# Performance work log

Measured on AMD Instinct MI355X. Metric: run time of the kernel, lower is better.

Reference implementation:

```python
import jax, jax.numpy as jnp
import numpy as np

CNT_R = 500
DIM = 128
B, NEI = 8192, 64


def setup_inputs() -> dict:
    key = jax.random.key(0)
    ks = jax.random.split(key, 10)
    d2 = 2 * DIM
    return {
        "batch_nei_e_emb": jax.random.normal(ks[0], (B, NEI, DIM), dtype=jnp.float32),
        "batch_nei_rw": jax.random.uniform(ks[1], (B, NEI), dtype=jnp.float32),
        "w_r_table": jax.random.normal(ks[2], (2 * CNT_R + 1, DIM), dtype=jnp.float32),
        "zq_table": jax.random.normal(ks[3], (2 * CNT_R, DIM), dtype=jnp.float32),
        "attn_W_w": jax.random.normal(ks[4], (d2, d2), dtype=jnp.float32) / np.sqrt(d2),
        "attn_W_b": jnp.zeros((d2,), dtype=jnp.float32),
        "u_a_w": jax.random.normal(ks[5], (d2,), dtype=jnp.float32) / np.sqrt(d2),
        "u_a_b": jnp.zeros((), dtype=jnp.float32),
        "batch_nei_rid": jax.random.randint(ks[6], (B, NEI), 0, 2 * CNT_R + 1),
        "batch_q_rid": jax.random.randint(ks[7], (B,), 0, 2 * CNT_R),
    }


def reference(batch_nei_e_emb, batch_nei_rw, w_r_table, zq_table,
              attn_W_w, attn_W_b, u_a_w, u_a_b,
              batch_nei_rid, batch_q_rid):
    # gather relation hyperplane normals: (B, NEI, DIM)
    w_r = w_r_table[batch_nei_rid]
    n = w_r / jnp.linalg.norm(w_r, axis=-1, keepdims=True)
    # hyperplane projection: e - (e . n) n
    e = batch_nei_e_emb
    e_proj = e - jnp.sum(e * n, axis=-1, keepdims=True) * n
    # query relation embedding, tiled over neighbors: (B, NEI, DIM)
    z_q = zq_table[batch_q_rid]  # (B, DIM)
    z_q = jnp.broadcast_to(z_q[:, None, :], e_proj.shape)
    concat = jnp.concatenate([z_q, e_proj], axis=-1)  # (B, NEI, 2*DIM)
    h = jnp.tanh(jnp.einsum('bni,oi->bno', concat, attn_W_w) + attn_W_b)
    _alpha = jnp.einsum('bni,i->bn', h, u_a_w) + u_a_b  # (B, NEI)
    alpha = jax.nn.softmax(_alpha, axis=-1)
    attn = alpha + batch_nei_rw
    return attn
```

## Files before the change

### kernel.cpp

```cpp
#include <hip/hip_runtime.h>
#include <hip/hip_bf16.h>

#define NB    8192
#define NEI   64
#define DIM   128
#define D2    256
#define NR_W  1001
#define NR_Z  1000
#define EPB_LD 136
#define BPB   2
#define C2L2E 2.8853900817779268f

typedef __attribute__((ext_vector_type(8))) short bf16x8;
typedef __attribute__((ext_vector_type(4))) float f32x4;

__device__ __forceinline__ ushort f2bf(float x) {
    union { float f; unsigned u; } c; c.f = x;
    unsigned u = c.u;
    return (ushort)((u + 0x7fffu + ((u >> 16) & 1u)) >> 16);
}

__device__ __forceinline__ unsigned pk2(float a, float b) {
    __hip_bfloat162 h = __float22bfloat162_rn(make_float2(a, b));
    return *(unsigned*)&h;
}


__global__ void k_norm(const float* __restrict__ w_r_table, float* __restrict__ norm_t) {
    int r = blockIdx.x;
    int t = threadIdx.x;
    float v = w_r_table[r * DIM + t];
    float s = v * v;
    #pragma unroll
    for (int m = 1; m < 64; m <<= 1) s += __shfl_xor(s, m);
    __shared__ float sh[2];
    if ((t & 63) == 0) sh[t >> 6] = s;
    __syncthreads();
    float tot = sh[0] + sh[1];
    norm_t[r * DIM + t] = v / sqrtf(tot);
}

__global__ void k_tq(const float* __restrict__ zq_table, const float* __restrict__ W,
                     const float* __restrict__ bias, float* __restrict__ tq_t) {
    int r = blockIdx.x;
    int o = threadIdx.x;
    __shared__ float4 z4[32];
    if (o < 32) z4[o] = ((const float4*)(zq_table + r * DIM))[o];
    __syncthreads();
    const float4* wr = (const float4*)(W + o * D2);
    float acc = bias[o];
    #pragma unroll 8
    for (int i = 0; i < 32; ++i) {
        float4 wv = wr[i], zv = z4[i];
        acc += wv.x*zv.x + wv.y*zv.y + wv.z*zv.z + wv.w*zv.w;
    }
    tq_t[r * D2 + o] = acc;
}

__global__ void k_bfrag(const float* __restrict__ W, ushort* __restrict__ bfrag) {
    int ot = blockIdx.x;
    int kt = blockIdx.y;
    int l  = threadIdx.x;
    int o  = ot * 16 + (l & 15);
    int k  = kt * 32 + (l >> 4) * 8;
    const float4* src = (const float4*)(W + o * D2 + DIM + k);
    float4 a = src[0], c = src[1];
    uint4 w;
    w.x = f2bf(a.x) | ((unsigned)f2bf(a.y) << 16);
    w.y = f2bf(a.z) | ((unsigned)f2bf(a.w) << 16);
    w.z = f2bf(c.x) | ((unsigned)f2bf(c.y) << 16);
    w.w = f2bf(c.z) | ((unsigned)f2bf(c.w) << 16);
    *(uint4*)(bfrag + ((ot * 4 + kt) * 64 + l) * 8) = w;
}

__global__ void k_sua(const float* __restrict__ u, float* __restrict__ sua) {
    int t = threadIdx.x;
    float v = u[t];
    #pragma unroll
    for (int m = 1; m < 64; m <<= 1) v += __shfl_xor(v, m);
    __shared__ float sh[4];
    if ((t & 63) == 0) sh[t >> 6] = v;
    __syncthreads();
    if (t == 0) sua[0] = sh[0] + sh[1] + sh[2] + sh[3];
}


__global__ __launch_bounds__(512, 4) void k_main(
    const float* __restrict__ e_emb,
    const float* __restrict__ rw,
    const int*   __restrict__ nei_rid,
    const int*   __restrict__ q_rid,
    const float* __restrict__ norm_t,
    const float* __restrict__ tq_t,
    const ushort* __restrict__ bfrag,
    const float* __restrict__ u_a_sum,
    const float* __restrict__ u_a_w,
    float* __restrict__ out)
{
    __shared__ __align__(16) ushort ep16[NEI * EPB_LD];
    __shared__ float alpw[8][NEI];

    const int t    = threadIdx.x;
    const int wave = t >> 6, lane = t & 63;
    const int ln   = lane & 15, hi = lane >> 4;
    const int row  = t >> 3, q3 = t & 7;
    const int b0   = blockIdx.x * BPB;

    bf16x8 bfr_[2][4];
    #pragma unroll
    for (int nt = 0; nt < 2; ++nt)
        #pragma unroll
        for (int kt = 0; kt < 4; ++kt)
            bfr_[nt][kt] = *(const bf16x8*)(bfrag + ((((wave*2+nt)*4 + kt)*64 + lane)*8));
    asm volatile("" : "+v"(bfr_[0][0]), "+v"(bfr_[0][1]), "+v"(bfr_[0][2]), "+v"(bfr_[0][3]),
                      "+v"(bfr_[1][0]), "+v"(bfr_[1][1]), "+v"(bfr_[1][2]), "+v"(bfr_[1][3]));
    float ua2[2];
    #pragma unroll
    for (int nt = 0; nt < 2; ++nt) ua2[nt] = u_a_w[wave*32 + nt*16 + ln];
    asm volatile("" : "+v"(ua2[0]), "+v"(ua2[1]));
    const float sua = u_a_sum[0];

    #pragma unroll 1
    for (int i = 0; i < BPB; ++i) {
        const int b = b0 + i;

        {
            const int rid = nei_rid[b * NEI + row];
            const float4* esrc = (const float4*)(e_emb + ((size_t)b * NEI + row) * DIM);
            const float4* nsrc = (const float4*)(norm_t + rid * DIM);
            float4 ev[4], nv[4];
            #pragma unroll
            for (int kk = 0; kk < 4; ++kk) {
                ev[kk] = esrc[q3 + 8*kk];
                nv[kk] = nsrc[q3 + 8*kk];
            }
            float part = 0.f;
            #pragma unroll
            for (int kk = 0; kk < 4; ++kk)
                part += ev[kk].x*nv[kk].x + ev[kk].y*nv[kk].y + ev[kk].z*nv[kk].z + ev[kk].w*nv[kk].w;
            part += __shfl_xor(part, 1);
            part += __shfl_xor(part, 2);
            part += __shfl_xor(part, 4);
            const float d = part;
            #pragma unroll
            for (int kk = 0; kk < 4; ++kk) {
                float p0 = fmaf(-d, nv[kk].x, ev[kk].x);
                float p1 = fmaf(-d, nv[kk].y, ev[kk].y);
                float p2 = fmaf(-d, nv[kk].z, ev[kk].z);
                float p3 = fmaf(-d, nv[kk].w, ev[kk].w);
                uint2 w2; w2.x = pk2(p0, p1); w2.y = pk2(p2, p3);
                *(uint2*)((char*)ep16 + row * (EPB_LD*2) + (q3 + 8*kk) * 8) = w2;
            }
        }

        float tq2[2];
        {
            int qr = q_rid[b];
            #pragma unroll
            for (int nt = 0; nt < 2; ++nt)
                tq2[nt] = C2L2E * tq_t[qr * D2 + wave*32 + nt*16 + ln];
        }

        __syncthreads();

        #pragma unroll
        for (int mt = 0; mt < 4; ++mt) {
            bf16x8 a_[4];
            #pragma unroll
            for (int kt = 0; kt < 4; ++kt)
                a_[kt] = *(const bf16x8*)&ep16[(mt*16 + ln) * EPB_LD + kt*32 + hi*8];
            f32x4 acc[2];
            #pragma unroll
            for (int nt = 0; nt < 2; ++nt) acc[nt] = (f32x4){0.f, 0.f, 0.f, 0.f};
            #pragma unroll
            for (int kt = 0; kt < 4; ++kt)
                #pragma unroll
                for (int nt = 0; nt < 2; ++nt)
                    acc[nt] = __builtin_amdgcn_mfma_f32_16x16x32_bf16(a_[kt], bfr_[nt][kt], acc[nt], 0, 0, 0);
            float pr[4] = {0.f, 0.f, 0.f, 0.f};
            #pragma unroll
            for (int nt = 0; nt < 2; ++nt)
                #pragma unroll
                for (int j = 0; j < 4; ++j) {
                    float e2 = __builtin_exp2f(fmaf(C2L2E, acc[nt][j], tq2[nt]));
                    float r  = __builtin_amdgcn_rcpf(e2 + 1.f);
                    pr[j] = fmaf(ua2[nt], r, pr[j]);
                }
            #pragma unroll
            for (int m = 1; m < 16; m <<= 1)
                #pragma unroll
                for (int j = 0; j < 4; ++j) pr[j] += __shfl_xor(pr[j], m);
            if (ln == 0) {
                #pragma unroll
                for (int j = 0; j < 4; ++j) alpw[wave][mt*16 + hi*4 + j] = pr[j];
            }
        }

        __syncthreads();

        if (t < NEI) {
            float s8 = 0.f;
            #pragma unroll
            for (int w = 0; w < 8; ++w) s8 += alpw[w][t];
            float a = fmaf(-2.f, s8, sua);
            float p = __expf(a);
            float s = p;
            #pragma unroll
            for (int m = 1; m < 64; m <<= 1) s += __shfl_xor(s, m);
            out[(size_t)b * NEI + t] = fmaf(p, __builtin_amdgcn_rcpf(s), rw[(size_t)b * NEI + t]);
        }
    }
}


extern "C" void kernel_launch(void* const* d_in, const int* in_sizes, int n_in,
                              void* d_out, int out_size, void* d_ws, size_t ws_size,
                              hipStream_t stream) {
    const float* e_emb   = (const float*)d_in[0];
    const float* rw      = (const float*)d_in[1];
    const float* w_r_tab = (const float*)d_in[2];
    const float* zq_tab  = (const float*)d_in[3];
    const float* attn_W  = (const float*)d_in[4];
    const float* attn_b  = (const float*)d_in[5];
    const float* u_a_w   = (const float*)d_in[6];
    const int*   nei_rid = (const int*)d_in[8];
    const int*   q_rid   = (const int*)d_in[9];
    float* out = (float*)d_out;

    float* ws = (float*)d_ws;
    float* norm_t = ws;
    float* tq_t   = norm_t + NR_W * DIM;
    ushort* bfrag = (ushort*)(tq_t + NR_Z * D2);
    float* suap   = (float*)(bfrag + 16*4*64*8);

    k_norm<<<NR_W, DIM, 0, stream>>>(w_r_tab, norm_t);
    k_tq<<<NR_Z, D2, 0, stream>>>(zq_tab, attn_W, attn_b, tq_t);
    k_bfrag<<<dim3(16, 4), 64, 0, stream>>>(attn_W, bfrag);
    k_sua<<<1, 256, 0, stream>>>(u_a_w, suap);
    k_main<<<NB / BPB, 512, 0, stream>>>(e_emb, rw, nei_rid, q_rid,
                                         norm_t, tq_t, bfrag, suap, u_a_w, out);
}
```

Baseline: 143.7 us.

## Issue all global loads up front with inline asm, one batch per block

Each block now handles one batch element instead of two. All global loads (B fragments, embeddings, normals, tq, u_a, rw) are issued together as dwordx4 inline-asm loads before a single vmcnt wait. This maximises memory-level parallelism and removes the serialized per-iteration load latency. Launch bounds drop to 2 waves-per-EU hint, which allows more registers but may lower occupancy, and block count doubles, adding launch/prologue overhead per batch.

```diff
diff --git a/kernel.cpp b/kernel.cpp
--- a/kernel.cpp
+++ b/kernel.cpp
@@ -8,11 +8,15 @@
 #define NR_W  1001
 #define NR_Z  1000
 #define EPB_LD 136
-#define BPB   2
 #define C2L2E 2.8853900817779268f
 
 typedef __attribute__((ext_vector_type(8))) short bf16x8;
 typedef __attribute__((ext_vector_type(4))) float f32x4;
+typedef __attribute__((ext_vector_type(4))) unsigned int u32x4;
+
+#define GLOAD16(dst, addr, OFF) \
+    asm volatile("global_load_dwordx4 %0, %1, off offset:" OFF \
+                 : "=v"(dst) : "v"(addr))
 
 __device__ __forceinline__ ushort f2bf(float x) {
     union { float f; unsigned u; } c; c.f = x;
@@ -23,6 +27,13 @@
 __device__ __forceinline__ unsigned pk2(float a, float b) {
     __hip_bfloat162 h = __float22bfloat162_rn(make_float2(a, b));
     return *(unsigned*)&h;
+}
+
+__device__ __forceinline__ bf16x8 asbf(u32x4 v) {
+    union { u32x4 a; bf16x8 b; } u; u.a = v; return u.b;
+}
+__device__ __forceinline__ float4 asf4(u32x4 v) {
+    union { u32x4 a; float4 b; } u; u.a = v; return u.b;
 }
 
 
@@ -85,7 +96,7 @@
 }
 
 
-__global__ __launch_bounds__(512, 4) void k_main(
+__global__ __launch_bounds__(512, 2) void k_main(
     const float* __restrict__ e_emb,
     const float* __restrict__ rw,
     const int*   __restrict__ nei_rid,
@@ -103,112 +114,128 @@
     const int t    = threadIdx.x;
     const int wave = t >> 6, lane = t & 63;
     const int ln   = lane & 15, hi = lane >> 4;
-    const int row  = t >> 3, q3 = t & 7;
-    const int b0   = blockIdx.x * BPB;
-
-    bf16x8 bfr_[2][4];
+    const int rgrp = t >> 4, q4 = t & 15;
+    const int b    = blockIdx.x;
+
+    const char* bb0 = (const char*)bfrag + (((wave * 2) * 4 * 64) + lane) * 16;
+    const char* bb1 = bb0 + 4096;
+    u32x4 bq0, bq1, bq2, bq3, bq4, bq5, bq6, bq7;
+    GLOAD16(bq0, bb0, "0");    GLOAD16(bq1, bb0, "1024");
+    GLOAD16(bq2, bb0, "2048"); GLOAD16(bq3, bb0, "3072");
+    GLOAD16(bq4, bb1, "0");    GLOAD16(bq5, bb1, "1024");
+    GLOAD16(bq6, bb1, "2048"); GLOAD16(bq7, bb1, "3072");
+
+    const int rid0 = nei_rid[b * NEI + rgrp];
+    const int rid1 = nei_rid[b * NEI + 32 + rgrp];
+    const char* ea = (const char*)(e_emb + ((size_t)b * NEI + rgrp) * DIM + q4 * 8);
+    const char* eb = (const char*)(e_emb + ((size_t)b * NEI + 32 + rgrp) * DIM + q4 * 8);
+    const char* na = (const char*)(norm_t + rid0 * DIM + q4 * 8);
+    const char* nb = (const char*)(norm_t + rid1 * DIM + q4 * 8);
+    u32x4 qea0, qea1, qeb0, qeb1, qna0, qna1, qnb0, qnb1;
+    GLOAD16(qea0, ea, "0");  GLOAD16(qea1, ea, "16");
+    GLOAD16(qeb0, eb, "0");  GLOAD16(qeb1, eb, "16");
+    GLOAD16(qna0, na, "0");  GLOAD16(qna1, na, "16");
+    GLOAD16(qnb0, nb, "0");  GLOAD16(qnb1, nb, "16");
+
+    const int qr = q_rid[b];
+    const float tq0 = tq_t[qr * D2 + wave * 32 + ln];
+    const float tq1 = tq_t[qr * D2 + wave * 32 + 16 + ln];
+    const float ua0 = u_a_w[wave * 32 + ln];
+    const float ua1 = u_a_w[wave * 32 + 16 + ln];
+    const float rwv = rw[(size_t)b * NEI + (t & 63)];
+    const float sua = u_a_sum[0];
+
+    asm volatile("s_waitcnt vmcnt(0)" ::: "memory");
+    __builtin_amdgcn_sched_barrier(0);
+
+    const float4 ea0 = asf4(qea0), ea1 = asf4(qea1);
+    const float4 eb0 = asf4(qeb0), eb1 = asf4(qeb1);
+    const float4 na0 = asf4(qna0), na1 = asf4(qna1);
+    const float4 nb0 = asf4(qnb0), nb1 = asf4(qnb1);
+
+    {
+        float part = ea0.x*na0.x + ea0.y*na0.y + ea0.z*na0.z + ea0.w*na0.w
+                   + ea1.x*na1.x + ea1.y*na1.y + ea1.z*na1.z + ea1.w*na1.w;
+        part += __shfl_xor(part, 1);
+        part += __shfl_xor(part, 2);
+        part += __shfl_xor(part, 4);
+        part += __shfl_xor(part, 8);
+        const float d = part;
+        float p0 = fmaf(-d, na0.x, ea0.x), p1 = fmaf(-d, na0.y, ea0.y);
+        float p2 = fmaf(-d, na0.z, ea0.z), p3 = fmaf(-d, na0.w, ea0.w);
+        float p4 = fmaf(-d, na1.x, ea1.x), p5 = fmaf(-d, na1.y, ea1.y);
+        float p6 = fmaf(-d, na1.z, ea1.z), p7 = fmaf(-d, na1.w, ea1.w);
+        uint4 w; w.x = pk2(p0,p1); w.y = pk2(p2,p3); w.z = pk2(p4,p5); w.w = pk2(p6,p7);
+        *(uint4*)((char*)ep16 + rgrp * (EPB_LD*2) + q4 * 16) = w;
+    }
+    {
+        float part = eb0.x*nb0.x + eb0.y*nb0.y + eb0.z*nb0.z + eb0.w*nb0.w
+                   + eb1.x*nb1.x + eb1.y*nb1.y + eb1.z*nb1.z + eb1.w*nb1.w;
+        part += __shfl_xor(part, 1);
+        part += __shfl_xor(part, 2);
+        part += __shfl_xor(part, 4);
+        part += __shfl_xor(part, 8);
+        const float d = part;
+        float p0 = fmaf(-d, nb0.x, eb0.x), p1 = fmaf(-d, nb0.y, eb0.y);
+        float p2 = fmaf(-d, nb0.z, eb0.z), p3 = fmaf(-d, nb0.w, eb0.w);
+        float p4 = fmaf(-d, nb1.x, eb1.x), p5 = fmaf(-d, nb1.y, eb1.y);
+        float p6 = fmaf(-d, nb1.z, eb1.z), p7 = fmaf(-d, nb1.w, eb1.w);
+        uint4 w; w.x = pk2(p0,p1); w.y = pk2(p2,p3); w.z = pk2(p4,p5); w.w = pk2(p6,p7);
+        *(uint4*)((char*)ep16 + (32 + rgrp) * (EPB_LD*2) + q4 * 16) = w;
+    }
+
+    __syncthreads();
+
+    const bf16x8 bf00 = asbf(bq0), bf01 = asbf(bq1), bf02 = asbf(bq2), bf03 = asbf(bq3);
+    const bf16x8 bf10 = asbf(bq4), bf11 = asbf(bq5), bf12 = asbf(bq6), bf13 = asbf(bq7);
+    const float tqs0 = C2L2E * tq0, tqs1 = C2L2E * tq1;
+
     #pragma unroll
-    for (int nt = 0; nt < 2; ++nt)
+    for (int mt = 0; mt < 4; ++mt) {
+        bf16x8 a_[4];
         #pragma unroll
         for (int kt = 0; kt < 4; ++kt)
-            bfr_[nt][kt] = *(const bf16x8*)(bfrag + ((((wave*2+nt)*4 + kt)*64 + lane)*8));
-    asm volatile("" : "+v"(bfr_[0][0]), "+v"(bfr_[0][1]), "+v"(bfr_[0][2]), "+v"(bfr_[0][3]),
-                      "+v"(bfr_[1][0]), "+v"(bfr_[1][1]), "+v"(bfr_[1][2]), "+v"(bfr_[1][3]));
-    float ua2[2];
-    #pragma unroll
-    for (int nt = 0; nt < 2; ++nt) ua2[nt] = u_a_w[wave*32 + nt*16 + ln];
-    asm volatile("" : "+v"(ua2[0]), "+v"(ua2[1]));
-    const float sua = u_a_sum[0];
-
-    #pragma unroll 1
-    for (int i = 0; i < BPB; ++i) {
-        const int b = b0 + i;
-
-        {
-            const int rid = nei_rid[b * NEI + row];
-            const float4* esrc = (const float4*)(e_emb + ((size_t)b * NEI + row) * DIM);
-            const float4* nsrc = (const float4*)(norm_t + rid * DIM);
-            float4 ev[4], nv[4];
+            a_[kt] = *(const bf16x8*)&ep16[(mt*16 + ln) * EPB_LD + kt*32 + hi*8];
+        f32x4 acc0 = (f32x4){0.f,0.f,0.f,0.f}, acc1 = (f32x4){0.f,0.f,0.f,0.f};
+        acc0 = __builtin_amdgcn_mfma_f32_16x16x32_bf16(a_[0], bf00, acc0, 0, 0, 0);
+        acc1 = __builtin_amdgcn_mfma_f32_16x16x32_bf16(a_[0], bf10, acc1, 0, 0, 0);
+        acc0 = __builtin_amdgcn_mfma_f32_16x16x32_bf16(a_[1], bf01, acc0, 0, 0, 0);
+        acc1 = __builtin_amdgcn_mfma_f32_16x16x32_bf16(a_[1], bf11, acc1, 0, 0, 0);
+        acc0 = __builtin_amdgcn_mfma_f32_16x16x32_bf16(a_[2], bf02, acc0, 0, 0, 0);
+        acc1 = __builtin_amdgcn_mfma_f32_16x16x32_bf16(a_[2], bf12, acc1, 0, 0, 0);
+        acc0 = __builtin_amdgcn_mfma_f32_16x16x32_bf16(a_[3], bf03, acc0, 0, 0, 0);
+        acc1 = __builtin_amdgcn_mfma_f32_16x16x32_bf16(a_[3], bf13, acc1, 0, 0, 0);
+        float pr[4];
+        #pragma unroll
+        for (int j = 0; j < 4; ++j) {
+            float ex0 = __builtin_exp2f(fmaf(C2L2E, acc0[j], tqs0));
+            float ex1 = __builtin_exp2f(fmaf(C2L2E, acc1[j], tqs1));
+            float r0  = __builtin_amdgcn_rcpf(ex0 + 1.f);
+            float r1  = __builtin_amdgcn_rcpf(ex1 + 1.f);
+            pr[j] = fmaf(ua0, r0, ua1 * r1);
+        }
+        #pragma unroll
+        for (int m = 1; m < 16; m <<= 1)
             #pragma unroll
-            for (int kk = 0; kk < 4; ++kk) {
-                ev[kk] = esrc[q3 + 8*kk];
-                nv[kk] = nsrc[q3 + 8*kk];
-            }
-            float part = 0.f;
+            for (int j = 0; j < 4; ++j) pr[j] += __shfl_xor(pr[j], m);
+        if (ln == 0) {
             #pragma unroll
-            for (int kk = 0; kk < 4; ++kk)
-                part += ev[kk].x*nv[kk].x + ev[kk].y*nv[kk].y + ev[kk].z*nv[kk].z + ev[kk].w*nv[kk].w;
-            part += __shfl_xor(part, 1);
-            part += __shfl_xor(part, 2);
-            part += __shfl_xor(part, 4);
-            const float d = part;
-            #pragma unroll
-            for (int kk = 0; kk < 4; ++kk) {
-                float p0 = fmaf(-d, nv[kk].x, ev[kk].x);
-                float p1 = fmaf(-d, nv[kk].y, ev[kk].y);
-                float p2 = fmaf(-d, nv[kk].z, ev[kk].z);
-                float p3 = fmaf(-d, nv[kk].w, ev[kk].w);
-                uint2 w2; w2.x = pk2(p0, p1); w2.y = pk2(p2, p3);
-                *(uint2*)((char*)ep16 + row * (EPB_LD*2) + (q3 + 8*kk) * 8) = w2;
-            }
+            for (int j = 0; j < 4; ++j) alpw[wave][mt*16 + hi*4 + j] = pr[j];
         }
-
-        float tq2[2];
-        {
-            int qr = q_rid[b];
-            #pragma unroll
-            for (int nt = 0; nt < 2; ++nt)
-                tq2[nt] = C2L2E * tq_t[qr * D2 + wave*32 + nt*16 + ln];
-        }
-
-        __syncthreads();
-
-        #pragma unroll
-        for (int mt = 0; mt < 4; ++mt) {
-            bf16x8 a_[4];
-            #pragma unroll
-            for (int kt = 0; kt < 4; ++kt)
-                a_[kt] = *(const bf16x8*)&ep16[(mt*16 + ln) * EPB_LD + kt*32 + hi*8];
-            f32x4 acc[2];
-            #pragma unroll
-            for (int nt = 0; nt < 2; ++nt) acc[nt] = (f32x4){0.f, 0.f, 0.f, 0.f};
-            #pragma unroll
-            for (int kt = 0; kt < 4; ++kt)
-                #pragma unroll
-                for (int nt = 0; nt < 2; ++nt)
-                    acc[nt] = __builtin_amdgcn_mfma_f32_16x16x32_bf16(a_[kt], bfr_[nt][kt], acc[nt], 0, 0, 0);
-            float pr[4] = {0.f, 0.f, 0.f, 0.f};
-            #pragma unroll
-            for (int nt = 0; nt < 2; ++nt)
-                #pragma unroll
-                for (int j = 0; j < 4; ++j) {
-                    float e2 = __builtin_exp2f(fmaf(C2L2E, acc[nt][j], tq2[nt]));
-                    float r  = __builtin_amdgcn_rcpf(e2 + 1.f);
-                    pr[j] = fmaf(ua2[nt], r, pr[j]);
-                }
-            #pragma unroll
-            for (int m = 1; m < 16; m <<= 1)
-                #pragma unroll
-                for (int j = 0; j < 4; ++j) pr[j] += __shfl_xor(pr[j], m);
-            if (ln == 0) {
-                #pragma unroll
-                for (int j = 0; j < 4; ++j) alpw[wave][mt*16 + hi*4 + j] = pr[j];
-            }
-        }
-
-        __syncthreads();
-
-        if (t < NEI) {
-            float s8 = 0.f;
-            #pragma unroll
-            for (int w = 0; w < 8; ++w) s8 += alpw[w][t];
-            float a = fmaf(-2.f, s8, sua);
-            float p = __expf(a);
-            float s = p;
-            #pragma unroll
-            for (int m = 1; m < 64; m <<= 1) s += __shfl_xor(s, m);
-            out[(size_t)b * NEI + t] = fmaf(p, __builtin_amdgcn_rcpf(s), rw[(size_t)b * NEI + t]);
-        }
+    }
+
+    __syncthreads();
+
+    if (t < NEI) {
+        float s8 = 0.f;
+        #pragma unroll
+        for (int w = 0; w < 8; ++w) s8 += alpw[w][t];
+        float a = fmaf(-2.f, s8, sua);
+        float p = __expf(a);
+        float s = p;
+        #pragma unroll
+        for (int m = 1; m < 64; m <<= 1) s += __shfl_xor(s, m);
+        out[(size_t)b * NEI + t] = fmaf(p, __builtin_amdgcn_rcpf(s), rwv);
     }
 }
 
@@ -237,6 +264,6 @@
     k_tq<<<NR_Z, D2, 0, stream>>>(zq_tab, attn_W, attn_b, tq_t);
     k_bfrag<<<dim3(16, 4), 64, 0, stream>>>(attn_W, bfrag);
     k_sua<<<1, 256, 0, stream>>>(u_a_w, suap);
-    k_main<<<NB / BPB, 512, 0, stream>>>(e_emb, rw, nei_rid, q_rid,
-                                         norm_t, tq_t, bfrag, suap, u_a_w, out);
-}
+    k_main<<<NB, 512, 0, stream>>>(e_emb, rw, nei_rid, q_rid,
+                                   norm_t, tq_t, bfrag, suap, u_a_w, out);
+}
```

New measurement: 135.8 us. 1.06x faster.

## Assign one batch item per wave and build MFMA A-fragments in registers

Applied to the files above, without the earlier changes.

Each wave now processes a whole batch item, with all 256 output columns, instead of eight waves sharing one item. The projected activations are built straight into MFMA A-fragments in registers, so the LDS staging buffer and both per-item block barriers go away. The full bf16 weight fragment set is copied once per block into 64KB of LDS and read per column tile. In exchange, e_emb and the normal rows are loaded twice (once for the dot product, once for the projection), and the large LDS footprint may limit how many blocks fit per CU.

```diff
diff --git a/kernel.cpp b/kernel.cpp
--- a/kernel.cpp
+++ b/kernel.cpp
@@ -7,8 +7,7 @@
 #define D2    256
 #define NR_W  1001
 #define NR_Z  1000
-#define EPB_LD 136
-#define BPB   2
+#define BPW   2
 #define C2L2E 2.8853900817779268f
 
 typedef __attribute__((ext_vector_type(8))) short bf16x8;
@@ -23,6 +22,10 @@
 __device__ __forceinline__ unsigned pk2(float a, float b) {
     __hip_bfloat162 h = __float22bfloat162_rn(make_float2(a, b));
     return *(unsigned*)&h;
+}
+
+__device__ __forceinline__ bf16x8 mkbf(unsigned a, unsigned b, unsigned c, unsigned d) {
+    union { uint4 u; bf16x8 v; } x; x.u = make_uint4(a, b, c, d); return x.v;
 }
 
 
@@ -58,10 +61,10 @@
 }
 
 __global__ void k_bfrag(const float* __restrict__ W, ushort* __restrict__ bfrag) {
-    int ot = blockIdx.x;
+    int nt = blockIdx.x;
     int kt = blockIdx.y;
     int l  = threadIdx.x;
-    int o  = ot * 16 + (l & 15);
+    int o  = nt * 16 + (l & 15);
     int k  = kt * 32 + (l >> 4) * 8;
     const float4* src = (const float4*)(W + o * D2 + DIM + k);
     float4 a = src[0], c = src[1];
@@ -70,7 +73,7 @@
     w.y = f2bf(a.z) | ((unsigned)f2bf(a.w) << 16);
     w.z = f2bf(c.x) | ((unsigned)f2bf(c.y) << 16);
     w.w = f2bf(c.z) | ((unsigned)f2bf(c.w) << 16);
-    *(uint4*)(bfrag + ((ot * 4 + kt) * 64 + l) * 8) = w;
+    *(uint4*)(bfrag + ((nt * 4 + kt) * 64 + l) * 8) = w;
 }
 
 __global__ void k_sua(const float* __restrict__ u, float* __restrict__ sua) {
@@ -97,118 +100,125 @@
     const float* __restrict__ u_a_w,
     float* __restrict__ out)
 {
-    __shared__ __align__(16) ushort ep16[NEI * EPB_LD];
-    __shared__ float alpw[8][NEI];
+    __shared__ __align__(16) ushort w2l[16 * 4 * 64 * 8];
 
     const int t    = threadIdx.x;
     const int wave = t >> 6, lane = t & 63;
     const int ln   = lane & 15, hi = lane >> 4;
-    const int row  = t >> 3, q3 = t & 7;
-    const int b0   = blockIdx.x * BPB;
-
-    bf16x8 bfr_[2][4];
-    #pragma unroll
-    for (int nt = 0; nt < 2; ++nt)
+
+    {
+        const uint4* src = (const uint4*)bfrag;
+        uint4* dst = (uint4*)w2l;
+        #pragma unroll
+        for (int i = 0; i < 8; ++i) dst[t + 512 * i] = src[t + 512 * i];
+    }
+    __syncthreads();
+
+    const float sua = u_a_sum[0];
+
+    #pragma unroll 1
+    for (int ib = 0; ib < BPW; ++ib) {
+        const int b = (blockIdx.x * 8 + wave) * BPW + ib;
+
+        int ridv[4];
+        #pragma unroll
+        for (int mt = 0; mt < 4; ++mt) ridv[mt] = nei_rid[b * NEI + mt * 16 + ln];
+        const int qr = q_rid[b];
+
+        const float* er[4];
+        const float* nr[4];
+        #pragma unroll
+        for (int mt = 0; mt < 4; ++mt) {
+            er[mt] = e_emb + ((size_t)b * NEI + mt * 16 + ln) * DIM + hi * 8;
+            nr[mt] = norm_t + ridv[mt] * DIM + hi * 8;
+        }
+
+        float dacc[4] = {0.f, 0.f, 0.f, 0.f};
         #pragma unroll
         for (int kt = 0; kt < 4; ++kt)
-            bfr_[nt][kt] = *(const bf16x8*)(bfrag + ((((wave*2+nt)*4 + kt)*64 + lane)*8));
-    asm volatile("" : "+v"(bfr_[0][0]), "+v"(bfr_[0][1]), "+v"(bfr_[0][2]), "+v"(bfr_[0][3]),
-                      "+v"(bfr_[1][0]), "+v"(bfr_[1][1]), "+v"(bfr_[1][2]), "+v"(bfr_[1][3]));
-    float ua2[2];
-    #pragma unroll
-    for (int nt = 0; nt < 2; ++nt) ua2[nt] = u_a_w[wave*32 + nt*16 + ln];
-    asm volatile("" : "+v"(ua2[0]), "+v"(ua2[1]));
-    const float sua = u_a_sum[0];
-
-    #pragma unroll 1
-    for (int i = 0; i < BPB; ++i) {
-        const int b = b0 + i;
-
-        {
-            const int rid = nei_rid[b * NEI + row];
-            const float4* esrc = (const float4*)(e_emb + ((size_t)b * NEI + row) * DIM);
-            const float4* nsrc = (const float4*)(norm_t + rid * DIM);
-            float4 ev[4], nv[4];
-            #pragma unroll
-            for (int kk = 0; kk < 4; ++kk) {
-                ev[kk] = esrc[q3 + 8*kk];
-                nv[kk] = nsrc[q3 + 8*kk];
+            #pragma unroll
+            for (int mt = 0; mt < 4; ++mt) {
+                float4 e0 = ((const float4*)(er[mt] + kt * 32))[0];
+                float4 e1 = ((const float4*)(er[mt] + kt * 32))[1];
+                float4 n0 = ((const float4*)(nr[mt] + kt * 32))[0];
+                float4 n1 = ((const float4*)(nr[mt] + kt * 32))[1];
+                dacc[mt] += e0.x*n0.x + e0.y*n0.y + e0.z*n0.z + e0.w*n0.w
+                          + e1.x*n1.x + e1.y*n1.y + e1.z*n1.z + e1.w*n1.w;
             }
-            float part = 0.f;
-            #pragma unroll
-            for (int kk = 0; kk < 4; ++kk)
-                part += ev[kk].x*nv[kk].x + ev[kk].y*nv[kk].y + ev[kk].z*nv[kk].z + ev[kk].w*nv[kk].w;
-            part += __shfl_xor(part, 1);
-            part += __shfl_xor(part, 2);
-            part += __shfl_xor(part, 4);
-            const float d = part;
-            #pragma unroll
-            for (int kk = 0; kk < 4; ++kk) {
-                float p0 = fmaf(-d, nv[kk].x, ev[kk].x);
-                float p1 = fmaf(-d, nv[kk].y, ev[kk].y);
-                float p2 = fmaf(-d, nv[kk].z, ev[kk].z);
-                float p3 = fmaf(-d, nv[kk].w, ev[kk].w);
-                uint2 w2; w2.x = pk2(p0, p1); w2.y = pk2(p2, p3);
-                *(uint2*)((char*)ep16 + row * (EPB_LD*2) + (q3 + 8*kk) * 8) = w2;
+        #pragma unroll
+        for (int mt = 0; mt < 4; ++mt) {
+            dacc[mt] += __shfl_xor(dacc[mt], 16);
+            dacc[mt] += __shfl_xor(dacc[mt], 32);
+        }
+
+        bf16x8 A[4][4];
+        #pragma unroll
+        for (int kt = 0; kt < 4; ++kt)
+            #pragma unroll
+            for (int mt = 0; mt < 4; ++mt) {
+                float4 e0 = ((const float4*)(er[mt] + kt * 32))[0];
+                float4 e1 = ((const float4*)(er[mt] + kt * 32))[1];
+                float4 n0 = ((const float4*)(nr[mt] + kt * 32))[0];
+                float4 n1 = ((const float4*)(nr[mt] + kt * 32))[1];
+                const float d = dacc[mt];
+                float p0 = fmaf(-d, n0.x, e0.x), p1 = fmaf(-d, n0.y, e0.y);
+                float p2 = fmaf(-d, n0.z, e0.z), p3 = fmaf(-d, n0.w, e0.w);
+                float p4 = fmaf(-d, n1.x, e1.x), p5 = fmaf(-d, n1.y, e1.y);
+                float p6 = fmaf(-d, n1.z, e1.z), p7 = fmaf(-d, n1.w, e1.w);
+                A[mt][kt] = mkbf(pk2(p0,p1), pk2(p2,p3), pk2(p4,p5), pk2(p6,p7));
             }
-        }
-
-        float tq2[2];
-        {
-            int qr = q_rid[b];
-            #pragma unroll
-            for (int nt = 0; nt < 2; ++nt)
-                tq2[nt] = C2L2E * tq_t[qr * D2 + wave*32 + nt*16 + ln];
-        }
-
-        __syncthreads();
-
-        #pragma unroll
-        for (int mt = 0; mt < 4; ++mt) {
-            bf16x8 a_[4];
-            #pragma unroll
-            for (int kt = 0; kt < 4; ++kt)
-                a_[kt] = *(const bf16x8*)&ep16[(mt*16 + ln) * EPB_LD + kt*32 + hi*8];
-            f32x4 acc[2];
-            #pragma unroll
-            for (int nt = 0; nt < 2; ++nt) acc[nt] = (f32x4){0.f, 0.f, 0.f, 0.f};
-            #pragma unroll
-            for (int kt = 0; kt < 4; ++kt)
+
+        float pr[4][4];
+        #pragma unroll
+        for (int mt = 0; mt < 4; ++mt)
+            #pragma unroll
+            for (int j = 0; j < 4; ++j) pr[mt][j] = 0.f;
+
+        #pragma unroll 1
+        for (int nt = 0; nt < 16; ++nt) {
+            const float tql = C2L2E * tq_t[qr * D2 + nt * 16 + ln];
+            const float ual = u_a_w[nt * 16 + ln];
+            f32x4 acc[4];
+            #pragma unroll
+            for (int mt = 0; mt < 4; ++mt) acc[mt] = (f32x4){0.f,0.f,0.f,0.f};
+            #pragma unroll
+            for (int kt = 0; kt < 4; ++kt) {
+                bf16x8 Bt = *(const bf16x8*)((const char*)w2l + (((nt*4 + kt)*64 + lane) << 4));
                 #pragma unroll
-                for (int nt = 0; nt < 2; ++nt)
-                    acc[nt] = __builtin_amdgcn_mfma_f32_16x16x32_bf16(a_[kt], bfr_[nt][kt], acc[nt], 0, 0, 0);
-            float pr[4] = {0.f, 0.f, 0.f, 0.f};
-            #pragma unroll
-            for (int nt = 0; nt < 2; ++nt)
+                for (int mt = 0; mt < 4; ++mt)
+                    acc[mt] = __builtin_amdgcn_mfma_f32_16x16x32_bf16(A[mt][kt], Bt, acc[mt], 0, 0, 0);
+            }
+            #pragma unroll
+            for (int mt = 0; mt < 4; ++mt)
                 #pragma unroll
                 for (int j = 0; j < 4; ++j) {
-                    float e2 = __builtin_exp2f(fmaf(C2L2E, acc[nt][j], tq2[nt]));
-                    float r  = __builtin_amdgcn_rcpf(e2 + 1.f);
-                    pr[j] = fmaf(ua2[nt], r, pr[j]);
+                    float ex = __builtin_exp2f(fmaf(C2L2E, acc[mt][j], tql));
+                    float r  = __builtin_amdgcn_rcpf(ex + 1.f);
+                    pr[mt][j] = fmaf(ual, r, pr[mt][j]);
                 }
-            #pragma unroll
-            for (int m = 1; m < 16; m <<= 1)
+        }
+
+        #pragma unroll
+        for (int m = 1; m < 16; m <<= 1)
+            #pragma unroll
+            for (int mt = 0; mt < 4; ++mt)
                 #pragma unroll
-                for (int j = 0; j < 4; ++j) pr[j] += __shfl_xor(pr[j], m);
-            if (ln == 0) {
-                #pragma unroll
-                for (int j = 0; j < 4; ++j) alpw[wave][mt*16 + hi*4 + j] = pr[j];
-            }
-        }
-
-        __syncthreads();
-
-        if (t < NEI) {
-            float s8 = 0.f;
-            #pragma unroll
-            for (int w = 0; w < 8; ++w) s8 += alpw[w][t];
-            float a = fmaf(-2.f, s8, sua);
-            float p = __expf(a);
-            float s = p;
-            #pragma unroll
-            for (int m = 1; m < 64; m <<= 1) s += __shfl_xor(s, m);
-            out[(size_t)b * NEI + t] = fmaf(p, __builtin_amdgcn_rcpf(s), rw[(size_t)b * NEI + t]);
-        }
+                for (int j = 0; j < 4; ++j) pr[mt][j] += __shfl_xor(pr[mt][j], m);
+
+        float mya = 0.f;
+        #pragma unroll
+        for (int mt = 0; mt < 4; ++mt)
+            #pragma unroll
+            for (int j = 0; j < 4; ++j)
+                if (ln == mt * 4 + j) mya = pr[mt][j];
+        float alpha = fmaf(-2.f, mya, sua);
+        float myex = __expf(alpha);
+        float s = myex;
+        #pragma unroll
+        for (int m = 1; m < 64; m <<= 1) s += __shfl_xor(s, m);
+        const int row = ((ln >> 2) * 16) + (hi * 4) + (ln & 3);
+        const float rwv = rw[(size_t)b * NEI + row];
+        out[(size_t)b * NEI + row] = fmaf(myex, __builtin_amdgcn_rcpf(s), rwv);
     }
 }
 
@@ -237,6 +247,6 @@
     k_tq<<<NR_Z, D2, 0, stream>>>(zq_tab, attn_W, attn_b, tq_t);
     k_bfrag<<<dim3(16, 4), 64, 0, stream>>>(attn_W, bfrag);
     k_sua<<<1, 256, 0, stream>>>(u_a_w, suap);
-    k_main<<<NB / BPB, 512, 0, stream>>>(e_emb, rw, nei_rid, q_rid,
-                                         norm_t, tq_t, bfrag, suap, u_a_w, out);
-}
+    k_main<<<NB / (8 * BPW), 512, 0, stream>>>(e_emb, rw, nei_rid, q_rid,
+                                               norm_t, tq_t, bfrag, suap, u_a_w, out);
+}
```

New measurement: 205.1 us. 42.7% more time.
